# Kernel optimization log

Measured on AMD Instinct MI355X. Metric: run time of the kernel, lower is better.

Reference implementation:

```python
import jax, jax.numpy as jnp
import numpy as np

THETA = 10000.0


def apply_rope(x, theta):
    # x: [batch, heads, seq, head_dim], head_dim even
    d = x.shape[-1]
    s = x.shape[-2]
    freqs = 1.0 / (theta ** (jnp.arange(0, d, 2, dtype=jnp.float32) / d))  # [d/2]
    pos = jnp.arange(s, dtype=jnp.float32)
    ang = pos[:, None] * freqs[None, :]          # [seq, d/2]
    cos, sin = jnp.cos(ang), jnp.sin(ang)
    x_even = x[..., 0::2]
    x_odd = x[..., 1::2]
    r_even = x_even * cos - x_odd * sin
    r_odd = x_even * sin + x_odd * cos
    # interleave back: [..., seq, d/2, 2] -> [..., seq, d]
    out = jnp.stack([r_even, r_odd], axis=-1).reshape(x.shape)
    return out


def setup_inputs() -> dict:
    key = jax.random.key(0)
    ks = jax.random.split(key, 5)
    B, S, D = 2, 2048, 1024
    scale = 1.0 / np.sqrt(D)
    return {
        "x": jax.random.normal(ks[0], (B, S, D), dtype=jnp.float32),
        "q_proj_weight": jax.random.normal(ks[1], (D, D), dtype=jnp.float32) * scale,
        "k_proj_weight": jax.random.normal(ks[2], (D, D), dtype=jnp.float32) * scale,
        "v_proj_weight": jax.random.normal(ks[3], (D, D), dtype=jnp.float32) * scale,
        "o_proj_weight": jax.random.normal(ks[4], (D, D), dtype=jnp.float32) * scale,
    }


def reference(x, q_proj_weight, k_proj_weight, v_proj_weight, o_proj_weight):
    B, S, D = x.shape
    H = 16
    hd = D // H
    # projections: weight is (d_out, d_in)
    q = jnp.einsum('bsd,ed->bse', x, q_proj_weight)
    k = jnp.einsum('bsd,ed->bse', x, k_proj_weight)
    v = jnp.einsum('bsd,ed->bse', x, v_proj_weight)
    # split heads -> [B, H, S, hd]
    q = q.reshape(B, S, H, hd).transpose(0, 2, 1, 3)
    k = k.reshape(B, S, H, hd).transpose(0, 2, 1, 3)
    v = v.reshape(B, S, H, hd).transpose(0, 2, 1, 3)
    q = apply_rope(q, THETA)
    k = apply_rope(k, THETA)
    scores = jnp.einsum('bhqd,bhkd->bhqk', q, k) / jnp.sqrt(jnp.float32(hd))
    causal = jnp.tril(jnp.ones((S, S), dtype=bool))
    scores = jnp.where(causal, scores, -jnp.inf)
    attn = jax.nn.softmax(scores, axis=-1)
    out = jnp.einsum('bhqk,bhkd->bhqd', attn, v)
    out = out.transpose(0, 2, 1, 3).reshape(B, S, D)
    return jnp.einsum('bsv,dv->bsd', out, o_proj_weight)
```

## Files before the change

### kernel.cpp

```cpp
#include <hip/hip_runtime.h>
#include <hip/hip_bf16.h>
#include <stdint.h>

typedef __attribute__((ext_vector_type(4))) float f32x4;
typedef __attribute__((ext_vector_type(8))) __bf16 bf16x8;
typedef __attribute__((ext_vector_type(4))) __bf16 bf16x4;

#define DEVI __device__ __forceinline__

static constexpr int S_  = 2048;
static constexpr int D_  = 1024;
static constexpr int H_  = 16;
static constexpr int HD_ = 64;
static constexpr int M_  = 2 * S_;
static constexpr float SCL2 = 0.18033688f;

DEVI void gload_lds16(const void* gsrc, void* ldst) {
  __builtin_amdgcn_global_load_lds(
      (__attribute__((address_space(1))) void*)(void*)gsrc,
      (__attribute__((address_space(3))) void*)ldst, 16, 0, 0);
}

DEVI float fexp2(float x) {
  float r;
  asm("v_exp_f32 %0, %1" : "=v"(r) : "v"(x));
  return r;
}

__global__ __launch_bounds__(256) void cvt_all_kernel(
    const float* __restrict__ x, const float* __restrict__ wq,
    const float* __restrict__ wk, const float* __restrict__ wv,
    const float* __restrict__ wo,
    __bf16* __restrict__ xb, __bf16* __restrict__ wqb,
    __bf16* __restrict__ wkb, __bf16* __restrict__ wvb,
    __bf16* __restrict__ wob, float* __restrict__ tab) {
  int blk = blockIdx.x;
  if (blk < 8192) {
    int i = blk * 256 + threadIdx.x;
    const float* src; __bf16* dst; int off;
    if (i < (1 << 20))                      { src = x;  dst = xb;  off = 0; }
    else if (i < (1 << 20) + (1 << 18))     { src = wq; dst = wqb; off = (1 << 20); }
    else if (i < (1 << 20) + 2 * (1 << 18)) { src = wk; dst = wkb; off = (1 << 20) + (1 << 18); }
    else if (i < (1 << 20) + 3 * (1 << 18)) { src = wv; dst = wvb; off = (1 << 20) + 2 * (1 << 18); }
    else                                    { src = wo; dst = wob; off = (1 << 20) + 3 * (1 << 18); }
    int j = i - off;
    float4 v = reinterpret_cast<const float4*>(src)[j];
    bf16x4 o;
    o[0] = (__bf16)v.x; o[1] = (__bf16)v.y; o[2] = (__bf16)v.z; o[3] = (__bf16)v.w;
    reinterpret_cast<bf16x4*>(dst)[j] = o;
  } else {
    int i = (blk - 8192) * 256 + threadIdx.x;
    int s = i >> 5, f = i & 31;
    float freq = powf(10000.0f, -(float)(2 * f) / (float)HD_);
    float ang = (float)s * freq;
    tab[2 * i]     = cosf(ang);
    tab[2 * i + 1] = sinf(ang);
  }
}

__global__ __launch_bounds__(512, 6) void gemm_qkv(
    const __bf16* __restrict__ A, const __bf16* __restrict__ W0,
    const __bf16* __restrict__ W1, const __bf16* __restrict__ W2,
    __bf16* __restrict__ Cq, __bf16* __restrict__ Ck, __bf16* __restrict__ Cvt,
    const float* __restrict__ tab) {
  __shared__ __attribute__((aligned(16))) __bf16 As[128 * 32];
  __shared__ __attribute__((aligned(16))) __bf16 Bs[128 * 32];
  const int tid  = threadIdx.x;
  const int lane = tid & 63;
  const int wv   = tid >> 6;
  const int wr   = wv >> 2;
  const int wc   = wv & 3;
  const int m0 = blockIdx.x * 128;
  const int n0 = blockIdx.y * 128;
  const int z  = blockIdx.z;
  const __bf16* W = (z == 0) ? W0 : (z == 1 ? W1 : W2);
  const int arow = lane & 15;
  const int kgrp = (lane >> 4) * 8;

  f32x4 acc[4][2];
#pragma unroll
  for (int i = 0; i < 4; i++)
#pragma unroll
    for (int j = 0; j < 2; j++) acc[i][j] = f32x4{0.f, 0.f, 0.f, 0.f};

  for (int k0 = 0; k0 < 1024; k0 += 32) {
    __syncthreads();
    {
      int c   = wv * 64 + lane;
      int row = c >> 2;
      int kc  = (c & 3) * 8;
      gload_lds16(A + (size_t)(m0 + row) * 1024 + k0 + kc, As + wv * 512);
      gload_lds16(W + (size_t)(n0 + row) * 1024 + k0 + kc, Bs + wv * 512);
    }
    asm volatile("s_waitcnt vmcnt(0)" ::: "memory");
    __syncthreads();
    bf16x8 af[4], bw[2];
#pragma unroll
    for (int i = 0; i < 4; i++)
      af[i] = *reinterpret_cast<const bf16x8*>(As + (wr * 64 + i * 16 + arow) * 32 + kgrp);
#pragma unroll
    for (int j = 0; j < 2; j++)
      bw[j] = *reinterpret_cast<const bf16x8*>(Bs + (wc * 32 + j * 16 + arow) * 32 + kgrp);
#pragma unroll
    for (int i = 0; i < 4; i++)
#pragma unroll
      for (int j = 0; j < 2; j++)
        acc[i][j] = __builtin_amdgcn_mfma_f32_16x16x32_bf16(af[i], bw[j], acc[i][j], 0, 0, 0);
  }

  if (z == 2) {
#pragma unroll
    for (int i = 0; i < 4; i++) {
      int m = m0 + wr * 64 + i * 16 + (lane >> 4) * 4;
      int bb = m >> 11, srow = m & (S_ - 1);
#pragma unroll
      for (int j = 0; j < 2; j++) {
        int n = n0 + wc * 32 + j * 16 + arow;
        int h = n >> 6, d = n & 63;
        bf16x4 o4;
#pragma unroll
        for (int r = 0; r < 4; r++) o4[r] = (__bf16)acc[i][j][r];
        *reinterpret_cast<bf16x4*>(
            Cvt + ((size_t)(bb * H_ + h) * HD_ + d) * S_ + srow) = o4;
      }
    }
  } else {
#pragma unroll
    for (int i = 0; i < 4; i++) {
#pragma unroll
      for (int j = 0; j < 2; j++) {
#pragma unroll
        for (int r = 0; r < 4; r++) {
          int m = m0 + wr * 64 + i * 16 + (lane >> 4) * 4 + r;
          int n = n0 + wc * 32 + j * 16 + arow;
          float v = acc[i][j][r];
          int bb = m >> 11, srow = m & (S_ - 1);
          int h = n >> 6, d = n & 63;
          size_t oidx = ((size_t)(bb * H_ + h) * S_ + srow) * HD_ + d;
          float other = __shfl_xor(v, 1, 64);
          int fq = d >> 1;
          float2 cssn = *reinterpret_cast<const float2*>(tab + (srow * 32 + fq) * 2);
          float rv = (d & 1) ? (other * cssn.y + v * cssn.x)
                             : (v * cssn.x - other * cssn.y);
          if (z == 0) rv *= SCL2;
          ((z == 0) ? Cq : Ck)[oidx] = (__bf16)rv;
        }
      }
    }
  }
}

__global__ __launch_bounds__(512, 4) void gemm_bt0(
    const __bf16* __restrict__ A, const __bf16* __restrict__ W0,
    float* __restrict__ Cf) {
  __shared__ __attribute__((aligned(16))) __bf16 As[128 * 32];
  __shared__ __attribute__((aligned(16))) __bf16 Bs[64 * 32];
  const int tid  = threadIdx.x;
  const int lane = tid & 63;
  const int wv   = tid >> 6;
  const int wr   = wv >> 1;
  const int wc   = wv & 1;
  const int m0 = blockIdx.x * 128;
  const int n0 = blockIdx.y * 64;
  const int arow = lane & 15;
  const int kgrp = (lane >> 4) * 8;

  f32x4 acc[2][2];
#pragma unroll
  for (int i = 0; i < 2; i++)
#pragma unroll
    for (int j = 0; j < 2; j++) acc[i][j] = f32x4{0.f, 0.f, 0.f, 0.f};

  for (int k0 = 0; k0 < 1024; k0 += 32) {
    __syncthreads();
    {
      int c   = wv * 64 + lane;
      int row = c >> 2;
      int kc  = (c & 3) * 8;
      gload_lds16(A + (size_t)(m0 + row) * 1024 + k0 + kc, As + wv * 512);
      if (wv < 4)
        gload_lds16(W0 + (size_t)(n0 + row) * 1024 + k0 + kc, Bs + wv * 512);
    }
    asm volatile("s_waitcnt vmcnt(0)" ::: "memory");
    __syncthreads();
    bf16x8 af[2], bw[2];
#pragma unroll
    for (int i = 0; i < 2; i++)
      af[i] = *reinterpret_cast<const bf16x8*>(As + (wr * 32 + i * 16 + arow) * 32 + kgrp);
#pragma unroll
    for (int j = 0; j < 2; j++)
      bw[j] = *reinterpret_cast<const bf16x8*>(Bs + (wc * 32 + j * 16 + arow) * 32 + kgrp);
#pragma unroll
    for (int i = 0; i < 2; i++)
#pragma unroll
      for (int j = 0; j < 2; j++)
        acc[i][j] = __builtin_amdgcn_mfma_f32_16x16x32_bf16(af[i], bw[j], acc[i][j], 0, 0, 0);
  }

#pragma unroll
  for (int i = 0; i < 2; i++)
#pragma unroll
    for (int j = 0; j < 2; j++)
#pragma unroll
      for (int r = 0; r < 4; r++) {
        int m = m0 + wr * 32 + i * 16 + (lane >> 4) * 4 + r;
        int n = n0 + wc * 32 + j * 16 + arow;
        Cf[(size_t)m * D_ + n] = acc[i][j][r];
      }
}

__global__ __launch_bounds__(256, 2) void attn_kernel(
    const __bf16* __restrict__ Q, const __bf16* __restrict__ K,
    const __bf16* __restrict__ Vt, __bf16* __restrict__ O) {
  __shared__ __attribute__((aligned(16))) __bf16 Ks[2][128 * 64];
  __shared__ __attribute__((aligned(16))) __bf16 Vs[2][64 * 128];
  const int tid = threadIdx.x, lane = tid & 63, wv = tid >> 6;
  const int bh = blockIdx.x;
  const int pr = blockIdx.y;
  const int b = bh >> 4, h = bh & 15;
  const __bf16* Qb  = Q  + (size_t)bh * S_ * HD_;
  const __bf16* Kb  = K  + (size_t)bh * S_ * HD_;
  const __bf16* Vtb = Vt + (size_t)bh * HD_ * S_;
  const int arow = lane & 15, g = lane >> 4;

#define STAGE(K0, BK_, BV_)                                                   \
  do {                                                                        \
    _Pragma("unroll") for (int j = 0; j < 4; ++j) {                           \
      int c = (wv * 4 + j) * 64 + lane;                    \
      int rowk = c >> 3, qqk = c & 7;                                         \
      int qsk = qqk ^ (rowk & 7);                                             \
      int ctp = rowk >> 4, rw = rowk & 15;                                    \
      int kph = ((ctp & 4) << 4) + ((ctp & 2) << 4) + ((ctp & 1) << 2)        \
                + ((rw >> 2) << 3) + (rw & 3);                                \
      gload_lds16(Kb + (size_t)((K0) + kph) * HD_ + qsk * 8,                  \
                  (BK_) + (size_t)(wv * 4 + j) * 512);                        \
      int rowv = c >> 4, qqv = c & 15;                                        \
      int qsv = qqv ^ (rowv & 7);                                             \
      gload_lds16(Vtb + (size_t)rowv * S_ + (K0) + qsv * 8,                   \
                  (BV_) + (size_t)(wv * 4 + j) * 512);                        \
    }                                                                         \
  } while (0)

  for (int seg = 0; seg < 2; ++seg) {
    const int qt = (seg == 0) ? pr : 31 - pr;
    const int q0 = qt * 64;
    const int nkv = (qt >> 1) + 1;
    const int qw = q0 + wv * 16;
    const int qg = qw + arow;

    bf16x8 aq[2];
#pragma unroll
    for (int j = 0; j < 2; j++)
      aq[j] = *reinterpret_cast<const bf16x8*>(
          Qb + (size_t)(qw + arow) * HD_ + j * 32 + g * 8);

    f32x4 po[4];
#pragma unroll
    for (int dt = 0; dt < 4; dt++) po[dt] = f32x4{0.f, 0.f, 0.f, 0.f};
    float mrow = -1e30f, lrow = 0.f;

    STAGE(0, Ks[0], Vs[0]);
    {
      int t1 = (nkv > 1) ? 128 : 0;
      STAGE(t1, Ks[1], Vs[1]);
    }
    asm volatile("s_waitcnt vmcnt(8)" ::: "memory");
    __builtin_amdgcn_s_barrier();

    for (int kt = 0; kt < nkv; ++kt) {
      const int k0 = kt * 128;
      const int cur = kt & 1;
      const __bf16* Kc = Ks[cur];
      const __bf16* Vc = Vs[cur];

      f32x4 sc4[8];
      __builtin_amdgcn_s_setprio(1);
#pragma unroll
      for (int ct = 0; ct < 8; ct++) {
        sc4[ct] = f32x4{0.f, 0.f, 0.f, 0.f};
        int L = ct * 16 + arow;
#pragma unroll
        for (int j2 = 0; j2 < 2; j2++) {
          int byt = (L * 128 + j2 * 64 + g * 16) ^ ((L & 7) << 4);
          bf16x8 kb = *reinterpret_cast<const bf16x8*>((const char*)Kc + byt);
          sc4[ct] = __builtin_amdgcn_mfma_f32_16x16x32_bf16(kb, aq[j2], sc4[ct], 0, 0, 0);
        }
      }
      __builtin_amdgcn_s_setprio(0);

      if (kt == nkv - 1) {
#pragma unroll
        for (int ct = 0; ct < 8; ct++) {
          int kb0 = k0 + ((ct & 4) << 4) + ((ct & 2) << 4) + ((ct & 1) << 2) + g * 8;
#pragma unroll
          for (int r = 0; r < 4; r++)
            if (kb0 + r > qg) sc4[ct][r] = -1e30f;
        }
      }

      float mx = -1e30f;
#pragma unroll
      for (int ct = 0; ct < 8; ct++)
#pragma unroll
        for (int r = 0; r < 4; r++) mx = fmaxf(mx, sc4[ct][r]);
      mx = fmaxf(mx, __shfl_xor(mx, 16, 64));
      mx = fmaxf(mx, __shfl_xor(mx, 32, 64));

      bool noskip = !__all(mx <= mrow + 11.0f);
      if (noskip) {
        float mnew = fmaxf(mrow, mx);
        float corr = fexp2(mrow - mnew);
        mrow = mnew;
        lrow *= corr;
#pragma unroll
        for (int dt = 0; dt < 4; dt++)
#pragma unroll
          for (int r = 0; r < 4; r++) po[dt][r] *= corr;
      }

      float rs = 0.f;
#pragma unroll
      for (int ct = 0; ct < 8; ct++)
#pragma unroll
        for (int r = 0; r < 4; r++) {
          float e = fexp2(sc4[ct][r] - mrow);
          sc4[ct][r] = e;
          rs += e;
        }
      rs += __shfl_xor(rs, 16, 64);
      rs += __shfl_xor(rs, 32, 64);
      lrow += rs;

      bf16x8 pb[4];
#pragma unroll
      for (int h2 = 0; h2 < 2; h2++)
#pragma unroll
        for (int j2 = 0; j2 < 2; j2++) {
#pragma unroll
          for (int r = 0; r < 4; r++) {
            pb[h2 * 2 + j2][r]     = (__bf16)sc4[h2 * 4 + 2 * j2][r];
            pb[h2 * 2 + j2][4 + r] = (__bf16)sc4[h2 * 4 + 2 * j2 + 1][r];
          }
        }

      __builtin_amdgcn_s_setprio(1);
#pragma unroll
      for (int dt = 0; dt < 4; dt++) {
        int d = dt * 16 + arow;
#pragma unroll
        for (int jj = 0; jj < 4; jj++) {
          int byv = (d * 256 + jj * 64 + g * 16) ^ ((d & 7) << 4);
          bf16x8 vb = *reinterpret_cast<const bf16x8*>((const char*)Vc + byv);
          po[dt] = __builtin_amdgcn_mfma_f32_16x16x32_bf16(vb, pb[jj], po[dt], 0, 0, 0);
        }
      }
      __builtin_amdgcn_s_setprio(0);

      __builtin_amdgcn_s_barrier();
      if (kt < nkv - 1) {
        int nx = kt + 2;
        if (nx > nkv - 1) nx = nkv - 1;
        STAGE(nx * 128, Ks[cur], Vs[cur]);
        asm volatile("s_waitcnt vmcnt(8)" ::: "memory");
      } else {
        asm volatile("s_waitcnt vmcnt(0)" ::: "memory");
      }
      __builtin_amdgcn_s_barrier();
    }

    float inv = __builtin_amdgcn_rcpf(lrow);
#pragma unroll
    for (int dt = 0; dt < 4; dt++) {
      bf16x4 o4;
#pragma unroll
      for (int r = 0; r < 4; r++) o4[r] = (__bf16)(po[dt][r] * inv);
      *reinterpret_cast<bf16x4*>(
          O + (size_t)(b * S_ + qg) * D_ + h * HD_ + dt * 16 + g * 4) = o4;
    }
  }
#undef STAGE
}

extern "C" void kernel_launch(void* const* d_in, const int* in_sizes, int n_in,
                              void* d_out, int out_size, void* d_ws, size_t ws_size,
                              hipStream_t stream) {
  const float* x  = (const float*)d_in[0];
  const float* wq = (const float*)d_in[1];
  const float* wk = (const float*)d_in[2];
  const float* wv = (const float*)d_in[3];
  const float* wo = (const float*)d_in[4];
  float* out = (float*)d_out;

  char* w = (char*)d_ws;
  __bf16* xb  = (__bf16*)(w);
  __bf16* wqb = (__bf16*)(w + (8u  << 20));
  __bf16* wkb = (__bf16*)(w + (10u << 20));
  __bf16* wvb = (__bf16*)(w + (12u << 20));
  __bf16* wob = (__bf16*)(w + (14u << 20));
  __bf16* qws = (__bf16*)(w + (16u << 20));
  __bf16* kws = (__bf16*)(w + (24u << 20));
  __bf16* vtw = (__bf16*)(w + (32u << 20));
  __bf16* aws = (__bf16*)(w + (40u << 20));
  float*  tab = (float*)(w + (48u << 20));

  cvt_all_kernel<<<8448, 256, 0, stream>>>(x, wq, wk, wv, wo,
                                           xb, wqb, wkb, wvb, wob, tab);
  gemm_qkv<<<dim3(32, 8, 3), 512, 0, stream>>>(xb, wqb, wkb, wvb,
                                               qws, kws, vtw, tab);
  attn_kernel<<<dim3(2 * H_, S_ / 128), 256, 0, stream>>>(qws, kws, vtw, aws);
  gemm_bt0<<<dim3(M_ / 128, D_ / 64), 512, 0, stream>>>(aws, wob, out);
}
```

Before: 106.7 us.

## Software-pipeline QK^T of next tile with softmax/PV of current tile

Restructures the attention inner loop so the QK^T MFMAs for tile kt+1 are issued before the softmax and PV of tile kt, using two score register sets and a loop unrolled by two. K gets a third LDS buffer and is prefetched one tile further ahead than V. The aim is to overlap matrix-core work with the exp/max VALU work. In exchange it uses more registers (a second set of 8 f32x4 scores) and more LDS, which could hurt occupancy at launch bounds (256,2). The buffer and wait-count bookkeeping is also more intricate.

```diff
diff --git a/kernel.cpp b/kernel.cpp
--- a/kernel.cpp
+++ b/kernel.cpp
@@ -212,7 +212,7 @@
 __global__ __launch_bounds__(256, 2) void attn_kernel(
     const __bf16* __restrict__ Q, const __bf16* __restrict__ K,
     const __bf16* __restrict__ Vt, __bf16* __restrict__ O) {
-  __shared__ __attribute__((aligned(16))) __bf16 Ks[2][128 * 64];
+  __shared__ __attribute__((aligned(16))) __bf16 Ks[3][128 * 64];
   __shared__ __attribute__((aligned(16))) __bf16 Vs[2][64 * 128];
   const int tid = threadIdx.x, lane = tid & 63, wv = tid >> 6;
   const int bh = blockIdx.x;
@@ -223,22 +223,101 @@
   const __bf16* Vtb = Vt + (size_t)bh * HD_ * S_;
   const int arow = lane & 15, g = lane >> 4;
 
-#define STAGE(K0, BK_, BV_)                                                   \
+#define STAGE_K(K0, DST)                                                      \
   do {                                                                        \
     _Pragma("unroll") for (int j = 0; j < 4; ++j) {                           \
-      int c = (wv * 4 + j) * 64 + lane;                    \
+      int c = (wv * 4 + j) * 64 + lane;                                       \
       int rowk = c >> 3, qqk = c & 7;                                         \
       int qsk = qqk ^ (rowk & 7);                                             \
       int ctp = rowk >> 4, rw = rowk & 15;                                    \
       int kph = ((ctp & 4) << 4) + ((ctp & 2) << 4) + ((ctp & 1) << 2)        \
                 + ((rw >> 2) << 3) + (rw & 3);                                \
       gload_lds16(Kb + (size_t)((K0) + kph) * HD_ + qsk * 8,                  \
-                  (BK_) + (size_t)(wv * 4 + j) * 512);                        \
+                  (DST) + (size_t)(wv * 4 + j) * 512);                        \
+    }                                                                         \
+  } while (0)
+
+#define STAGE_V(K0, DST)                                                      \
+  do {                                                                        \
+    _Pragma("unroll") for (int j = 0; j < 4; ++j) {                           \
+      int c = (wv * 4 + j) * 64 + lane;                                       \
       int rowv = c >> 4, qqv = c & 15;                                        \
       int qsv = qqv ^ (rowv & 7);                                             \
       gload_lds16(Vtb + (size_t)rowv * S_ + (K0) + qsv * 8,                   \
-                  (BV_) + (size_t)(wv * 4 + j) * 512);                        \
-    }                                                                         \
+                  (DST) + (size_t)(wv * 4 + j) * 512);                        \
+    }                                                                         \
+  } while (0)
+
+#define QKT(KC, SC)                                                           \
+  do {                                                                        \
+    __builtin_amdgcn_s_setprio(1);                                            \
+    _Pragma("unroll") for (int ct = 0; ct < 8; ct++) {                        \
+      (SC)[ct] = f32x4{0.f, 0.f, 0.f, 0.f};                                   \
+      int L = ct * 16 + arow;                                                 \
+      _Pragma("unroll") for (int j2 = 0; j2 < 2; j2++) {                      \
+        int byt = (L * 128 + j2 * 64 + g * 16) ^ ((L & 7) << 4);              \
+        bf16x8 kb = *reinterpret_cast<const bf16x8*>((const char*)(KC) + byt);\
+        (SC)[ct] = __builtin_amdgcn_mfma_f32_16x16x32_bf16(kb, aq[j2],        \
+                                                           (SC)[ct], 0, 0, 0);\
+      }                                                                       \
+    }                                                                         \
+    __builtin_amdgcn_s_setprio(0);                                            \
+  } while (0)
+
+#define SMPV(KT, SC, VC)                                                      \
+  do {                                                                        \
+    const int k0_ = (KT) * 128;                                               \
+    if ((KT) == nkv - 1) {                                                    \
+      _Pragma("unroll") for (int ct = 0; ct < 8; ct++) {                      \
+        int kb0 = k0_ + ((ct & 4) << 4) + ((ct & 2) << 4) + ((ct & 1) << 2)   \
+                  + g * 8;                                                    \
+        _Pragma("unroll") for (int r = 0; r < 4; r++)                         \
+          if (kb0 + r > qg) (SC)[ct][r] = -1e30f;                             \
+      }                                                                       \
+    }                                                                         \
+    float mx = -1e30f;                                                        \
+    _Pragma("unroll") for (int ct = 0; ct < 8; ct++)                          \
+      _Pragma("unroll") for (int r = 0; r < 4; r++)                           \
+        mx = fmaxf(mx, (SC)[ct][r]);                                          \
+    mx = fmaxf(mx, __shfl_xor(mx, 16, 64));                                   \
+    mx = fmaxf(mx, __shfl_xor(mx, 32, 64));                                   \
+    bool noskip = !__all(mx <= mrow + 11.0f);                                 \
+    if (noskip) {                                                             \
+      float mnew = fmaxf(mrow, mx);                                           \
+      float corr = fexp2(mrow - mnew);                                        \
+      mrow = mnew;                                                            \
+      lrow *= corr;                                                           \
+      _Pragma("unroll") for (int dt = 0; dt < 4; dt++)                        \
+        _Pragma("unroll") for (int r = 0; r < 4; r++) po[dt][r] *= corr;      \
+    }                                                                         \
+    float rs = 0.f;                                                           \
+    _Pragma("unroll") for (int ct = 0; ct < 8; ct++)                          \
+      _Pragma("unroll") for (int r = 0; r < 4; r++) {                         \
+        float e = fexp2((SC)[ct][r] - mrow);                                  \
+        (SC)[ct][r] = e;                                                      \
+        rs += e;                                                              \
+      }                                                                       \
+    rs += __shfl_xor(rs, 16, 64);                                             \
+    rs += __shfl_xor(rs, 32, 64);                                             \
+    lrow += rs;                                                               \
+    bf16x8 pb[4];                                                             \
+    _Pragma("unroll") for (int h2 = 0; h2 < 2; h2++)                          \
+      _Pragma("unroll") for (int j2 = 0; j2 < 2; j2++)                        \
+        _Pragma("unroll") for (int r = 0; r < 4; r++) {                       \
+          pb[h2 * 2 + j2][r]     = (__bf16)(SC)[h2 * 4 + 2 * j2][r];          \
+          pb[h2 * 2 + j2][4 + r] = (__bf16)(SC)[h2 * 4 + 2 * j2 + 1][r];      \
+        }                                                                     \
+    __builtin_amdgcn_s_setprio(1);                                            \
+    _Pragma("unroll") for (int dt = 0; dt < 4; dt++) {                        \
+      int d = dt * 16 + arow;                                                 \
+      _Pragma("unroll") for (int jj = 0; jj < 4; jj++) {                      \
+        int byv = (d * 256 + jj * 64 + g * 16) ^ ((d & 7) << 4);              \
+        bf16x8 vb = *reinterpret_cast<const bf16x8*>((const char*)(VC) + byv);\
+        po[dt] = __builtin_amdgcn_mfma_f32_16x16x32_bf16(vb, pb[jj],          \
+                                                         po[dt], 0, 0, 0);    \
+      }                                                                       \
+    }                                                                         \
+    __builtin_amdgcn_s_setprio(0);                                            \
   } while (0)
 
   for (int seg = 0; seg < 2; ++seg) {
@@ -258,114 +337,52 @@
 #pragma unroll
     for (int dt = 0; dt < 4; dt++) po[dt] = f32x4{0.f, 0.f, 0.f, 0.f};
     float mrow = -1e30f, lrow = 0.f;
-
-    STAGE(0, Ks[0], Vs[0]);
+    f32x4 scA[8], scB[8];
+
+    STAGE_K(0, Ks[0]);
+    STAGE_V(0, Vs[0]);
     {
       int t1 = (nkv > 1) ? 128 : 0;
-      STAGE(t1, Ks[1], Vs[1]);
+      STAGE_K(t1, Ks[1]);
+      STAGE_V(t1, Vs[1]);
+      int t2 = (nkv > 2) ? 256 : t1;
+      STAGE_K(t2, Ks[2]);
     }
     asm volatile("s_waitcnt vmcnt(8)" ::: "memory");
     __builtin_amdgcn_s_barrier();
 
-    for (int kt = 0; kt < nkv; ++kt) {
-      const int k0 = kt * 128;
-      const int cur = kt & 1;
-      const __bf16* Kc = Ks[cur];
-      const __bf16* Vc = Vs[cur];
-
-      f32x4 sc4[8];
-      __builtin_amdgcn_s_setprio(1);
-#pragma unroll
-      for (int ct = 0; ct < 8; ct++) {
-        sc4[ct] = f32x4{0.f, 0.f, 0.f, 0.f};
-        int L = ct * 16 + arow;
-#pragma unroll
-        for (int j2 = 0; j2 < 2; j2++) {
-          int byt = (L * 128 + j2 * 64 + g * 16) ^ ((L & 7) << 4);
-          bf16x8 kb = *reinterpret_cast<const bf16x8*>((const char*)Kc + byt);
-          sc4[ct] = __builtin_amdgcn_mfma_f32_16x16x32_bf16(kb, aq[j2], sc4[ct], 0, 0, 0);
-        }
-      }
-      __builtin_amdgcn_s_setprio(0);
-
-      if (kt == nkv - 1) {
-#pragma unroll
-        for (int ct = 0; ct < 8; ct++) {
-          int kb0 = k0 + ((ct & 4) << 4) + ((ct & 2) << 4) + ((ct & 1) << 2) + g * 8;
-#pragma unroll
-          for (int r = 0; r < 4; r++)
-            if (kb0 + r > qg) sc4[ct][r] = -1e30f;
-        }
-      }
-
-      float mx = -1e30f;
-#pragma unroll
-      for (int ct = 0; ct < 8; ct++)
-#pragma unroll
-        for (int r = 0; r < 4; r++) mx = fmaxf(mx, sc4[ct][r]);
-      mx = fmaxf(mx, __shfl_xor(mx, 16, 64));
-      mx = fmaxf(mx, __shfl_xor(mx, 32, 64));
-
-      bool noskip = !__all(mx <= mrow + 11.0f);
-      if (noskip) {
-        float mnew = fmaxf(mrow, mx);
-        float corr = fexp2(mrow - mnew);
-        mrow = mnew;
-        lrow *= corr;
-#pragma unroll
-        for (int dt = 0; dt < 4; dt++)
-#pragma unroll
-          for (int r = 0; r < 4; r++) po[dt][r] *= corr;
-      }
-
-      float rs = 0.f;
-#pragma unroll
-      for (int ct = 0; ct < 8; ct++)
-#pragma unroll
-        for (int r = 0; r < 4; r++) {
-          float e = fexp2(sc4[ct][r] - mrow);
-          sc4[ct][r] = e;
-          rs += e;
-        }
-      rs += __shfl_xor(rs, 16, 64);
-      rs += __shfl_xor(rs, 32, 64);
-      lrow += rs;
-
-      bf16x8 pb[4];
-#pragma unroll
-      for (int h2 = 0; h2 < 2; h2++)
-#pragma unroll
-        for (int j2 = 0; j2 < 2; j2++) {
-#pragma unroll
-          for (int r = 0; r < 4; r++) {
-            pb[h2 * 2 + j2][r]     = (__bf16)sc4[h2 * 4 + 2 * j2][r];
-            pb[h2 * 2 + j2][4 + r] = (__bf16)sc4[h2 * 4 + 2 * j2 + 1][r];
-          }
-        }
-
-      __builtin_amdgcn_s_setprio(1);
-#pragma unroll
-      for (int dt = 0; dt < 4; dt++) {
-        int d = dt * 16 + arow;
-#pragma unroll
-        for (int jj = 0; jj < 4; jj++) {
-          int byv = (d * 256 + jj * 64 + g * 16) ^ ((d & 7) << 4);
-          bf16x8 vb = *reinterpret_cast<const bf16x8*>((const char*)Vc + byv);
-          po[dt] = __builtin_amdgcn_mfma_f32_16x16x32_bf16(vb, pb[jj], po[dt], 0, 0, 0);
-        }
-      }
-      __builtin_amdgcn_s_setprio(0);
-
+    QKT(Ks[0], scA);
+
+    for (int kt = 0; kt < nkv; kt += 2) {
+      if (kt + 1 < nkv) QKT(Ks[(kt + 1) % 3], scB);
+      SMPV(kt, scA, Vs[0]);
       __builtin_amdgcn_s_barrier();
       if (kt < nkv - 1) {
-        int nx = kt + 2;
-        if (nx > nkv - 1) nx = nkv - 1;
-        STAGE(nx * 128, Ks[cur], Vs[cur]);
+        int tk = (kt + 3 <= nkv - 1) ? kt + 3 : nkv - 1;
+        int tv = (kt + 2 <= nkv - 1) ? kt + 2 : nkv - 1;
+        STAGE_K(tk * 128, Ks[(kt + 3) % 3]);
+        STAGE_V(tv * 128, Vs[0]);
         asm volatile("s_waitcnt vmcnt(8)" ::: "memory");
       } else {
         asm volatile("s_waitcnt vmcnt(0)" ::: "memory");
       }
       __builtin_amdgcn_s_barrier();
+
+      if (kt + 1 < nkv) {
+        if (kt + 2 < nkv) QKT(Ks[(kt + 2) % 3], scA);
+        SMPV(kt + 1, scB, Vs[1]);
+        __builtin_amdgcn_s_barrier();
+        if (kt + 1 < nkv - 1) {
+          int tk = (kt + 4 <= nkv - 1) ? kt + 4 : nkv - 1;
+          int tv = (kt + 3 <= nkv - 1) ? kt + 3 : nkv - 1;
+          STAGE_K(tk * 128, Ks[(kt + 4) % 3]);
+          STAGE_V(tv * 128, Vs[1]);
+          asm volatile("s_waitcnt vmcnt(8)" ::: "memory");
+        } else {
+          asm volatile("s_waitcnt vmcnt(0)" ::: "memory");
+        }
+        __builtin_amdgcn_s_barrier();
+      }
     }
 
     float inv = __builtin_amdgcn_rcpf(lrow);
@@ -378,7 +395,10 @@
           O + (size_t)(b * S_ + qg) * D_ + h * HD_ + dt * 16 + g * 4) = o4;
     }
   }
-#undef STAGE
+#undef STAGE_K
+#undef STAGE_V
+#undef QKT
+#undef SMPV
 }
 
 extern "C" void kernel_launch(void* const* d_in, const int* in_sizes, int n_in,
```

Measured after the change: 109.1 us. 1.02x slower.
